# Optimization experiments

Measured on AMD Instinct MI355X. Metric: run time of the kernel, lower is better.

Reference implementation:

```python
import jax, jax.numpy as jnp
import numpy as np

D, H, E, C, B = 1024, 2048, 8, 1024, 8192


def setup_inputs() -> dict:
    key = jax.random.key(0)
    ks = jax.random.split(key, 12)
    s_d = 1.0 / np.sqrt(D)
    s_h = 1.0 / np.sqrt(H)
    return {
        "x": jax.random.normal(ks[0], (B, D), dtype=jnp.float32),
        # gate (Router): Linear(D,D) -> relu -> Linear(D,E) -> softmax
        "gate_w1": jax.random.normal(ks[1], (D, D), dtype=jnp.float32) * s_d,
        "gate_b1": jax.random.normal(ks[2], (D,), dtype=jnp.float32) * s_d,
        "gate_w2": jax.random.normal(ks[3], (D, E), dtype=jnp.float32) * s_d,
        "gate_b2": jax.random.normal(ks[4], (E,), dtype=jnp.float32) * s_d,
        # experts stacked: fc1 [E,D,H], fc2 [E,H,H]
        "W1": jax.random.normal(ks[5], (E, D, H), dtype=jnp.float32) * s_d,
        "b1": jax.random.normal(ks[6], (E, H), dtype=jnp.float32) * s_d,
        "W2": jax.random.normal(ks[7], (E, H, H), dtype=jnp.float32) * s_h,
        "b2": jax.random.normal(ks[8], (E, H), dtype=jnp.float32) * s_h,
        # classifier Linear(H, C)
        "clf_w": jax.random.normal(ks[9], (H, C), dtype=jnp.float32) * s_h,
        "clf_b": jax.random.normal(ks[10], (C,), dtype=jnp.float32) * s_h,
    }


def reference(x, gate_w1, gate_b1, gate_w2, gate_b2, W1, b1, W2, b2, clf_w, clf_b):
    # Router: softmax over experts (dim=1)
    g = jax.nn.relu(x @ gate_w1 + gate_b1)          # [B, D]
    scores = jax.nn.softmax(g @ gate_w2 + gate_b2, axis=1)  # [B, E]

    # All experts, dense (training-mode forward): batched GEMMs over E
    h = jax.nn.relu(jnp.einsum('bd,edh->beh', x, W1) + b1[None])   # [B, E, H]
    expert_outs = jnp.einsum('beh,ehk->bek', h, W2) + b2[None]      # [B, E, H]

    # Shared classifier applied per (token, expert)
    logits = jnp.einsum('beh,hc->bec', expert_outs, clf_w) + clf_b  # [B, E, C]
    return logits, scores
```

## Files before the change

### kernel.cpp

```cpp
#include <hip/hip_runtime.h>
#include <stdint.h>

#define B_DIM 8192
#define D_DIM 1024
#define H_DIM 2048
#define E_DIM 8
#define C_DIM 1024

typedef _Float16 f16x8 __attribute__((ext_vector_type(8)));
typedef float f32x4 __attribute__((ext_vector_type(4)));

__device__ __forceinline__ void store_val(float* p, float v) { *p = v; }
__device__ __forceinline__ void store_val(_Float16* p, float v) { *p = (_Float16)v; }

__device__ __forceinline__ void async_cp16(const void* g, void* l) {
  __builtin_amdgcn_global_load_lds((const __attribute__((address_space(1))) void*)g,
                                   (__attribute__((address_space(3))) void*)l, 16, 0, 0);
}

template <bool RELU, bool BIAS, typename OUT_T>
__global__ void __launch_bounds__(256) gemm_bt(
    const _Float16* __restrict__ A, long aZ,
    const _Float16* __restrict__ Bt, long bZ,
    const float* __restrict__ bias, long biasZ,
    OUT_T* __restrict__ out, long outZ,
    int K, long rs)
{
  __shared__ _Float16 ldsA[128 * 64];
  __shared__ _Float16 ldsB[128 * 64];

  const int z = blockIdx.z;
  A   += (size_t)z * aZ;
  Bt  += (size_t)z * bZ;
  if (BIAS) bias += (size_t)z * biasZ;
  out += (size_t)z * outZ;

  const int tid  = threadIdx.x;
  const int wave = tid >> 6;
  const int lane = tid & 63;
  const int q    = lane >> 4;
  const int l16  = lane & 15;
  const int l8   = lane >> 3;
  const int l7   = lane & 7;

  const int m0   = blockIdx.y * 128;
  const int n0   = blockIdx.x * 128;
  const int wrow = (wave >> 1) * 64;
  const int wcol = (wave & 1) * 64;

  const int swz_st = ((l7 ^ l8) << 3);
  const _Float16* pa[4];
  const _Float16* pb[4];
#pragma unroll
  for (int i = 0; i < 4; ++i) {
    int ci = wave * 4 + i;
    pa[i] = A  + (size_t)(m0 + ci * 8 + l8) * K + swz_st;
    pb[i] = Bt + (size_t)(n0 + ci * 8 + l8) * K + swz_st;
  }

  int a_off[2][4], b_off[2][4];
#pragma unroll
  for (int kk = 0; kk < 2; ++kk) {
#pragma unroll
    for (int r = 0; r < 4; ++r) {
      int sw = ((kk * 4 + q) ^ (l16 & 7)) << 4;
      a_off[kk][r] = (wrow + r * 16 + l16) * 128 + sw;
      b_off[kk][r] = (wcol + r * 16 + l16) * 128 + sw;
    }
  }

  f32x4 acc[4][4];
#pragma unroll
  for (int r = 0; r < 4; ++r)
#pragma unroll
    for (int c = 0; c < 4; ++c)
      acc[r][c] = (f32x4){0.f, 0.f, 0.f, 0.f};

  const char* lAc = (const char*)ldsA;
  const char* lBc = (const char*)ldsB;

  for (int kt = 0; kt < K; kt += 64) {
    __syncthreads();
#pragma unroll
    for (int i = 0; i < 4; ++i) {
      int ci = wave * 4 + i;
      async_cp16(pa[i], ldsA + ci * 512);
      async_cp16(pb[i], ldsB + ci * 512);
      pa[i] += 64;
      pb[i] += 64;
    }
    __syncthreads();
#pragma unroll
    for (int kk = 0; kk < 2; ++kk) {
      f16x8 af[4], bfv[4];
#pragma unroll
      for (int r = 0; r < 4; ++r) af[r]  = *(const f16x8*)(lAc + a_off[kk][r]);
#pragma unroll
      for (int c = 0; c < 4; ++c) bfv[c] = *(const f16x8*)(lBc + b_off[kk][c]);
#pragma unroll
      for (int r = 0; r < 4; ++r)
#pragma unroll
        for (int c = 0; c < 4; ++c)
          acc[r][c] = __builtin_amdgcn_mfma_f32_16x16x32_f16(af[r], bfv[c], acc[r][c], 0, 0, 0);
    }
  }

#pragma unroll
  for (int c = 0; c < 4; ++c) {
    int col = n0 + wcol + c * 16 + l16;
    float bv = BIAS ? bias[col] : 0.f;
#pragma unroll
    for (int r = 0; r < 4; ++r) {
      int row = m0 + wrow + r * 16 + q * 4;
      f32x4 v = acc[r][c];
#pragma unroll
      for (int i = 0; i < 4; ++i) {
        float xv = v[i] + bv;
        if (RELU) xv = fmaxf(xv, 0.f);
        store_val(out + (size_t)(row + i) * rs + col, xv);
      }
    }
  }
}

template <bool RELU, bool BIAS, typename OUT_T, int K_CT>
__global__ void __launch_bounds__(512) gemm256(
    const _Float16* __restrict__ A, long aZ,
    const _Float16* __restrict__ Bt, long bZ,
    const float* __restrict__ bias, long biasZ,
    OUT_T* __restrict__ out, long outZ, long rs)
{
  constexpr int NT = K_CT / 64;
  __shared__ _Float16 ldsA[2 * 256 * 64];
  __shared__ _Float16 ldsB[2 * 256 * 64];

  const int z = blockIdx.z;
  A   += (size_t)z * aZ;
  Bt  += (size_t)z * bZ;
  if (BIAS) bias += (size_t)z * biasZ;
  out += (size_t)z * outZ;

  const int nwg = gridDim.x * gridDim.y;
  const int wg  = blockIdx.y * gridDim.x + blockIdx.x;
  const int sw  = (wg & 7) * (nwg >> 3) + (wg >> 3);
  const int bx  = sw % gridDim.x;
  const int by  = sw / gridDim.x;

  const int tid  = threadIdx.x;
  const int wave = tid >> 6;
  const int lane = tid & 63;
  const int q    = lane >> 4;
  const int l16  = lane & 15;
  const int l8   = lane >> 3;
  const int l7   = lane & 7;

  const int m0   = by * 256;
  const int n0   = bx * 256;
  const int wm   = wave >> 2;
  const int wn   = wave & 3;
  const int wrow = wm * 128;
  const int wcol = wn * 64;

  const int swz_st = ((l7 ^ l8) << 3);
  const _Float16* paB = A  + (size_t)(m0 + wave * 16 + l8) * K_CT + swz_st;
  const _Float16* pbB = Bt + (size_t)(n0 + wave * 16 + l8) * K_CT + swz_st;

  int a_base[2], b_base[2];
#pragma unroll
  for (int kk = 0; kk < 2; ++kk) {
    int swr = (((kk * 4 + q) ^ (l16 & 7)) << 4);
    a_base[kk] = (wrow + l16) * 128 + swr;
    b_base[kk] = (wcol + l16) * 128 + swr;
  }

  f32x4 acc[8][4];
#pragma unroll
  for (int r = 0; r < 8; ++r)
#pragma unroll
    for (int c = 0; c < 4; ++c)
      acc[r][c] = (f32x4){0.f, 0.f, 0.f, 0.f};

  const char* lA = (const char*)ldsA;
  const char* lB = (const char*)ldsB;

#define STAGE_A(bufe, hh, ptr)                                                        \
  {                                                                                   \
    _Pragma("unroll")                                                                 \
    for (int i_ = 0; i_ < 2; ++i_)                                                    \
      async_cp16((ptr) + (size_t)((hh) * 128 + i_ * 8) * K_CT,                        \
                 (void*)(ldsA + (bufe) + (hh) * 8192 + (wave * 2 + i_) * 512));       \
  }
#define STAGE_B(bufe, hh, ptr)                                                        \
  {                                                                                   \
    _Pragma("unroll")                                                                 \
    for (int i_ = 0; i_ < 2; ++i_)                                                    \
      async_cp16((ptr) + (size_t)((hh) * 128 + i_ * 8) * K_CT,                        \
                 (void*)(ldsB + (bufe) + (hh) * 8192 + (wave * 2 + i_) * 512));       \
  }

  STAGE_A(0, 0, paB) STAGE_A(0, 1, paB)
  STAGE_B(0, 0, pbB) STAGE_B(0, 1, pbB)
  STAGE_B(16384, 0, pbB + 64) STAGE_B(16384, 1, pbB + 64)
  asm volatile("s_waitcnt vmcnt(4)" ::: "memory");
  __builtin_amdgcn_s_barrier();

  const _Float16* pa_t = paB + 64;
  const _Float16* pb_t = pbB + 128;

  for (int t = 0; t < NT; ++t) {
    const int bofs  = (t & 1) * 32768;
    const int nbufe = ((t + 1) & 1) * 16384;
    const int cbufe = (t & 1) * 16384;
    f16x8 bf[4];
#pragma unroll
    for (int p = 0; p < 4; ++p) {
      const int kk = p >> 1, h = p & 1;
      if (h == 0) {
#pragma unroll
        for (int c = 0; c < 4; ++c)
          bf[c] = *(const f16x8*)(lB + bofs + b_base[kk] + c * 2048);
      }
      f16x8 af[4];
#pragma unroll
      for (int r = 0; r < 4; ++r)
        af[r] = *(const f16x8*)(lA + bofs + a_base[kk] + (h * 4 + r) * 2048);

      if (p == 0 && t + 1 < NT) STAGE_A(nbufe, 0, pa_t)
      if (p == 1 && t + 1 < NT) STAGE_A(nbufe, 1, pa_t)
      if (p == 3 && t + 2 < NT) { STAGE_B(cbufe, 0, pb_t) STAGE_B(cbufe, 1, pb_t) }

      __builtin_amdgcn_s_setprio(1);
#pragma unroll
      for (int c = 0; c < 4; ++c)
#pragma unroll
        for (int r = 0; r < 4; ++r)
          acc[h * 4 + r][c] = __builtin_amdgcn_mfma_f32_16x16x32_f16(
              af[r], bf[c], acc[h * 4 + r][c], 0, 0, 0);
      __builtin_amdgcn_s_setprio(0);

      if (p == 3) {
        if (t < NT - 2) asm volatile("s_waitcnt vmcnt(4)" ::: "memory");
        else            asm volatile("s_waitcnt vmcnt(0)" ::: "memory");
      }
      __builtin_amdgcn_s_barrier();
    }
    pa_t += 64;
    pb_t += 64;
  }
#undef STAGE_A
#undef STAGE_B

#pragma unroll
  for (int c = 0; c < 4; ++c) {
    int col = n0 + wcol + c * 16 + l16;
    float bv = BIAS ? bias[col] : 0.f;
#pragma unroll
    for (int r = 0; r < 8; ++r) {
      int row = m0 + wrow + r * 16 + q * 4;
      f32x4 v = acc[r][c];
#pragma unroll
      for (int i = 0; i < 4; ++i) {
        float xv = v[i] + bv;
        if (RELU) xv = fmaxf(xv, 0.f);
        store_val(out + (size_t)(row + i) * rs + col, xv);
      }
    }
  }
}

__global__ void cast_f32_f16(const float* __restrict__ in, _Float16* __restrict__ out, int n) {
  int i = (blockIdx.x * blockDim.x + threadIdx.x) * 4;
  if (i >= n) return;
  float4 v = *(const float4*)(in + i);
  union { _Float16 h[4]; uint2 u; } r;
  r.h[0] = (_Float16)v.x; r.h[1] = (_Float16)v.y;
  r.h[2] = (_Float16)v.z; r.h[3] = (_Float16)v.w;
  *(uint2*)(out + i) = r.u;
}

__global__ void transpose_cast(const float* __restrict__ in, _Float16* __restrict__ out,
                               int R, int Cn) {
  __shared__ float tile[32][33];
  in  += (size_t)blockIdx.z * R * Cn;
  out += (size_t)blockIdx.z * R * Cn;
  int c0 = blockIdx.x * 32, r0 = blockIdx.y * 32;
  int tx = threadIdx.x, ty = threadIdx.y;
#pragma unroll
  for (int i = ty; i < 32; i += 8)
    tile[i][tx] = in[(size_t)(r0 + i) * Cn + c0 + tx];
  __syncthreads();
#pragma unroll
  for (int i = ty; i < 32; i += 8)
    out[(size_t)(c0 + i) * R + r0 + tx] = (_Float16)tile[tx][i];
}

__global__ void gate2_softmax(const _Float16* __restrict__ g, const float* __restrict__ w2,
                              const float* __restrict__ b2, float* __restrict__ scores) {
  int b = blockIdx.x;
  int t = threadIdx.x;
  int e = t >> 5, slice = t & 31;
  const _Float16* gr = g + (size_t)b * D_DIM;
  float acc = 0.f;
  for (int d0 = slice * 8; d0 < D_DIM; d0 += 256) {
    f16x8 gv = *(const f16x8*)(gr + d0);
#pragma unroll
    for (int j = 0; j < 8; ++j)
      acc += (float)gv[j] * w2[(d0 + j) * 8 + e];
  }
  __shared__ float red[256];
  red[t] = acc;
  __syncthreads();
  for (int ss = 16; ss > 0; ss >>= 1) {
    if (slice < ss) red[t] += red[t + ss];
    __syncthreads();
  }
  __shared__ float sm[8];
  if (slice == 0) sm[e] = red[t] + b2[e];
  __syncthreads();
  if (t == 0) {
    float mx = sm[0];
#pragma unroll
    for (int i = 1; i < 8; ++i) mx = fmaxf(mx, sm[i]);
    float ex[8], sum = 0.f;
#pragma unroll
    for (int i = 0; i < 8; ++i) { ex[i] = expf(sm[i] - mx); sum += ex[i]; }
    float inv = 1.f / sum;
#pragma unroll
    for (int i = 0; i < 8; ++i) scores[(size_t)b * 8 + i] = ex[i] * inv;
  }
}

__global__ void combined_bias(const float* __restrict__ b2, const float* __restrict__ cw,
                              const float* __restrict__ cb, float* __restrict__ bc) {
  int e  = blockIdx.y;
  int cl = threadIdx.x & 63;
  int c  = blockIdx.x * 64 + cl;
  int ks = threadIdx.x >> 6;
  float acc = 0.f;
  for (int k = ks; k < H_DIM; k += 4)
    acc += b2[e * H_DIM + k] * cw[(size_t)k * C_DIM + c];
  __shared__ float red[256];
  red[threadIdx.x] = acc;
  __syncthreads();
  if (ks == 0)
    bc[(size_t)e * C_DIM + c] = red[cl] + red[cl + 64] + red[cl + 128] + red[cl + 192] + cb[c];
}

extern "C" void kernel_launch(void* const* d_in, const int* in_sizes, int n_in,
                              void* d_out, int out_size, void* d_ws, size_t ws_size,
                              hipStream_t stream) {
  const float* x   = (const float*)d_in[0];
  const float* gw1 = (const float*)d_in[1];
  const float* gb1 = (const float*)d_in[2];
  const float* gw2 = (const float*)d_in[3];
  const float* gb2 = (const float*)d_in[4];
  const float* W1  = (const float*)d_in[5];
  const float* b1  = (const float*)d_in[6];
  const float* W2  = (const float*)d_in[7];
  const float* b2  = (const float*)d_in[8];
  const float* cw  = (const float*)d_in[9];
  const float* cb  = (const float*)d_in[10];

  char* ws = (char*)d_ws;
  _Float16* xb     = (_Float16*)(ws);
  _Float16* g      = (_Float16*)(ws + 16777216ull);
  _Float16* gw1t   = (_Float16*)(ws + 33554432ull);
  _Float16* W1t    = (_Float16*)(ws + 35651584ull);
  _Float16* W2c    = (_Float16*)(ws + 69206016ull);
  _Float16* cwt    = (_Float16*)(ws + 136314880ull);
  _Float16* WcombT = (_Float16*)(ws + 140509184ull);
  float*    bc     = (float*)   (ws + 174063616ull);
  _Float16* h_all  = (_Float16*)(ws + 174096384ull);

  float* logits = (float*)d_out;
  float* scores = logits + (size_t)B_DIM * E_DIM * C_DIM;

  cast_f32_f16<<<B_DIM * D_DIM / 4 / 256, 256, 0, stream>>>(x, xb, B_DIM * D_DIM);
  transpose_cast<<<dim3(32, 32, 1), dim3(32, 8), 0, stream>>>(gw1, gw1t, D_DIM, D_DIM);
  transpose_cast<<<dim3(64, 32, 8), dim3(32, 8), 0, stream>>>(W1, W1t, D_DIM, H_DIM);
  cast_f32_f16<<<E_DIM * H_DIM * H_DIM / 4 / 256, 256, 0, stream>>>(W2, W2c, E_DIM * H_DIM * H_DIM);
  transpose_cast<<<dim3(32, 64, 1), dim3(32, 8), 0, stream>>>(cw, cwt, H_DIM, C_DIM);

  gemm_bt<true, true, _Float16><<<dim3(8, 64, 1), 256, 0, stream>>>(
      xb, 0, gw1t, 0, gb1, 0, g, 0, D_DIM, (long)D_DIM);
  gate2_softmax<<<B_DIM, 256, 0, stream>>>(g, gw2, gb2, scores);

  gemm256<false, false, _Float16, H_DIM><<<dim3(8, 4, 8), 512, 0, stream>>>(
      cwt, 0, W2c, (long)H_DIM * H_DIM, nullptr, 0,
      WcombT, (long)C_DIM * H_DIM, (long)H_DIM);
  combined_bias<<<dim3(C_DIM / 64, E_DIM), 256, 0, stream>>>(b2, cw, cb, bc);

  gemm256<true, true, _Float16, D_DIM><<<dim3(8, 32, 8), 512, 0, stream>>>(
      xb, 0, W1t, (long)H_DIM * D_DIM, b1, (long)H_DIM,
      h_all, (long)B_DIM * H_DIM, (long)H_DIM);

  gemm256<false, true, float, H_DIM><<<dim3(4, 32, 8), 512, 0, stream>>>(
      h_all, (long)B_DIM * H_DIM, WcombT, (long)C_DIM * H_DIM, bc, (long)C_DIM,
      logits, (long)C_DIM, (long)(E_DIM * C_DIM));
}
```

Baseline: 1.469 ms.

## Restructure gemm256 main loop with register double-buffered fragments; warp-per-row gate softmax

The gemm256 K-loop is reorganised so that A/B fragments for the next K-slice are preloaded into registers while the current MFMAs run. Both A and B of the next tile are now staged once per iteration into a double buffer, replacing the prior three-deep B prefetch, with a full vmcnt(0) wait before the last barrier. Separately, gate2_softmax is rewritten to use one wavefront per token with shuffle reductions instead of a 256-thread shared-memory tree per token. The goal is to hide LDS read latency behind MFMAs and cut barrier and launch overhead in the router. The trade-off is higher register pressure and a shallower global prefetch.

After: 1.443 ms. Within noise of the previous version (-1.7%).

```diff
diff --git a/kernel.cpp b/kernel.cpp
--- a/kernel.cpp
+++ b/kernel.cpp
@@ -200,50 +200,76 @@
 
   STAGE_A(0, 0, paB) STAGE_A(0, 1, paB)
   STAGE_B(0, 0, pbB) STAGE_B(0, 1, pbB)
-  STAGE_B(16384, 0, pbB + 64) STAGE_B(16384, 1, pbB + 64)
-  asm volatile("s_waitcnt vmcnt(4)" ::: "memory");
+  asm volatile("s_waitcnt vmcnt(0)" ::: "memory");
   __builtin_amdgcn_s_barrier();
 
+  f16x8 afA[4], afB[4], bfv0[4], bfv1[4];
+#pragma unroll
+  for (int r = 0; r < 4; ++r) afA[r]  = *(const f16x8*)(lA + a_base[0] + r * 2048);
+#pragma unroll
+  for (int c = 0; c < 4; ++c) bfv0[c] = *(const f16x8*)(lB + b_base[0] + c * 2048);
+
   const _Float16* pa_t = paB + 64;
-  const _Float16* pb_t = pbB + 128;
+  const _Float16* pb_t = pbB + 64;
 
   for (int t = 0; t < NT; ++t) {
     const int bofs  = (t & 1) * 32768;
+    const int nofs  = bofs ^ 32768;
     const int nbufe = ((t + 1) & 1) * 16384;
-    const int cbufe = (t & 1) * 16384;
-    f16x8 bf[4];
-#pragma unroll
-    for (int p = 0; p < 4; ++p) {
-      const int kk = p >> 1, h = p & 1;
-      if (h == 0) {
-#pragma unroll
-        for (int c = 0; c < 4; ++c)
-          bf[c] = *(const f16x8*)(lB + bofs + b_base[kk] + c * 2048);
-      }
-      f16x8 af[4];
+
+#pragma unroll
+    for (int r = 0; r < 4; ++r) afB[r]  = *(const f16x8*)(lA + bofs + a_base[1] + r * 2048);
+#pragma unroll
+    for (int c = 0; c < 4; ++c) bfv1[c] = *(const f16x8*)(lB + bofs + b_base[1] + c * 2048);
+    if (t + 1 < NT) { STAGE_A(nbufe, 0, pa_t) STAGE_A(nbufe, 1, pa_t) }
+    __builtin_amdgcn_s_setprio(1);
+#pragma unroll
+    for (int c = 0; c < 4; ++c)
 #pragma unroll
       for (int r = 0; r < 4; ++r)
-        af[r] = *(const f16x8*)(lA + bofs + a_base[kk] + (h * 4 + r) * 2048);
-
-      if (p == 0 && t + 1 < NT) STAGE_A(nbufe, 0, pa_t)
-      if (p == 1 && t + 1 < NT) STAGE_A(nbufe, 1, pa_t)
-      if (p == 3 && t + 2 < NT) { STAGE_B(cbufe, 0, pb_t) STAGE_B(cbufe, 1, pb_t) }
-
-      __builtin_amdgcn_s_setprio(1);
-#pragma unroll
-      for (int c = 0; c < 4; ++c)
-#pragma unroll
-        for (int r = 0; r < 4; ++r)
-          acc[h * 4 + r][c] = __builtin_amdgcn_mfma_f32_16x16x32_f16(
-              af[r], bf[c], acc[h * 4 + r][c], 0, 0, 0);
-      __builtin_amdgcn_s_setprio(0);
-
-      if (p == 3) {
-        if (t < NT - 2) asm volatile("s_waitcnt vmcnt(4)" ::: "memory");
-        else            asm volatile("s_waitcnt vmcnt(0)" ::: "memory");
-      }
-      __builtin_amdgcn_s_barrier();
-    }
+        acc[r][c] = __builtin_amdgcn_mfma_f32_16x16x32_f16(afA[r], bfv0[c], acc[r][c], 0, 0, 0);
+    __builtin_amdgcn_s_setprio(0);
+    __builtin_amdgcn_s_barrier();
+
+#pragma unroll
+    for (int r = 0; r < 4; ++r) afA[r] = *(const f16x8*)(lA + bofs + a_base[0] + (4 + r) * 2048);
+    if (t + 1 < NT) { STAGE_B(nbufe, 0, pb_t) STAGE_B(nbufe, 1, pb_t) }
+    __builtin_amdgcn_s_setprio(1);
+#pragma unroll
+    for (int c = 0; c < 4; ++c)
+#pragma unroll
+      for (int r = 0; r < 4; ++r)
+        acc[r][c] = __builtin_amdgcn_mfma_f32_16x16x32_f16(afB[r], bfv1[c], acc[r][c], 0, 0, 0);
+    __builtin_amdgcn_s_setprio(0);
+    __builtin_amdgcn_s_barrier();
+
+#pragma unroll
+    for (int r = 0; r < 4; ++r) afB[r] = *(const f16x8*)(lA + bofs + a_base[1] + (4 + r) * 2048);
+    __builtin_amdgcn_s_setprio(1);
+#pragma unroll
+    for (int c = 0; c < 4; ++c)
+#pragma unroll
+      for (int r = 0; r < 4; ++r)
+        acc[4 + r][c] = __builtin_amdgcn_mfma_f32_16x16x32_f16(afA[r], bfv0[c], acc[4 + r][c], 0, 0, 0);
+    __builtin_amdgcn_s_setprio(0);
+    asm volatile("s_waitcnt vmcnt(0)" ::: "memory");
+    __builtin_amdgcn_s_barrier();
+
+    if (t + 1 < NT) {
+#pragma unroll
+      for (int r = 0; r < 4; ++r) afA[r]  = *(const f16x8*)(lA + nofs + a_base[0] + r * 2048);
+#pragma unroll
+      for (int c = 0; c < 4; ++c) bfv0[c] = *(const f16x8*)(lB + nofs + b_base[0] + c * 2048);
+    }
+    __builtin_amdgcn_s_setprio(1);
+#pragma unroll
+    for (int c = 0; c < 4; ++c)
+#pragma unroll
+      for (int r = 0; r < 4; ++r)
+        acc[4 + r][c] = __builtin_amdgcn_mfma_f32_16x16x32_f16(afB[r], bfv1[c], acc[4 + r][c], 0, 0, 0);
+    __builtin_amdgcn_s_setprio(0);
+    __builtin_amdgcn_s_barrier();
+
     pa_t += 64;
     pb_t += 64;
   }
@@ -296,37 +322,40 @@
 
 __global__ void gate2_softmax(const _Float16* __restrict__ g, const float* __restrict__ w2,
                               const float* __restrict__ b2, float* __restrict__ scores) {
-  int b = blockIdx.x;
-  int t = threadIdx.x;
-  int e = t >> 5, slice = t & 31;
+  int wv   = threadIdx.x >> 6;
+  int lane = threadIdx.x & 63;
+  int b    = blockIdx.x * 4 + wv;
   const _Float16* gr = g + (size_t)b * D_DIM;
-  float acc = 0.f;
-  for (int d0 = slice * 8; d0 < D_DIM; d0 += 256) {
+  float acc[8];
+#pragma unroll
+  for (int e = 0; e < 8; ++e) acc[e] = 0.f;
+#pragma unroll
+  for (int half = 0; half < 2; ++half) {
+    int d0 = lane * 8 + half * 512;
     f16x8 gv = *(const f16x8*)(gr + d0);
 #pragma unroll
-    for (int j = 0; j < 8; ++j)
-      acc += (float)gv[j] * w2[(d0 + j) * 8 + e];
-  }
-  __shared__ float red[256];
-  red[t] = acc;
-  __syncthreads();
-  for (int ss = 16; ss > 0; ss >>= 1) {
-    if (slice < ss) red[t] += red[t + ss];
-    __syncthreads();
-  }
-  __shared__ float sm[8];
-  if (slice == 0) sm[e] = red[t] + b2[e];
-  __syncthreads();
-  if (t == 0) {
-    float mx = sm[0];
-#pragma unroll
-    for (int i = 1; i < 8; ++i) mx = fmaxf(mx, sm[i]);
+    for (int j = 0; j < 8; ++j) {
+      float gx = (float)gv[j];
+#pragma unroll
+      for (int e = 0; e < 8; ++e) acc[e] += gx * w2[(d0 + j) * 8 + e];
+    }
+  }
+#pragma unroll
+  for (int s = 32; s > 0; s >>= 1)
+#pragma unroll
+    for (int e = 0; e < 8; ++e) acc[e] += __shfl_xor(acc[e], s);
+  if (lane == 0) {
+    float mx = acc[0] + b2[0];
+    float v[8];
+    v[0] = mx;
+#pragma unroll
+    for (int e = 1; e < 8; ++e) { v[e] = acc[e] + b2[e]; mx = fmaxf(mx, v[e]); }
     float ex[8], sum = 0.f;
 #pragma unroll
-    for (int i = 0; i < 8; ++i) { ex[i] = expf(sm[i] - mx); sum += ex[i]; }
+    for (int e = 0; e < 8; ++e) { ex[e] = expf(v[e] - mx); sum += ex[e]; }
     float inv = 1.f / sum;
 #pragma unroll
-    for (int i = 0; i < 8; ++i) scores[(size_t)b * 8 + i] = ex[i] * inv;
+    for (int e = 0; e < 8; ++e) scores[(size_t)b * 8 + e] = ex[e] * inv;
   }
 }
 
@@ -383,7 +412,7 @@
 
   gemm_bt<true, true, _Float16><<<dim3(8, 64, 1), 256, 0, stream>>>(
       xb, 0, gw1t, 0, gb1, 0, g, 0, D_DIM, (long)D_DIM);
-  gate2_softmax<<<B_DIM, 256, 0, stream>>>(g, gw2, gb2, scores);
+  gate2_softmax<<<B_DIM / 4, 256, 0, stream>>>(g, gw2, gb2, scores);
 
   gemm256<false, false, _Float16, H_DIM><<<dim3(8, 4, 8), 512, 0, stream>>>(
       cwt, 0, W2c, (long)H_DIM * H_DIM, nullptr, 0,
```
